# Kernel optimization log

Hardware: AMD Instinct MI355X
Metric: run time of the kernel (lower is better)

The kernel has to match this reference:

```python
import jax, jax.numpy as jnp
import numpy as np

N_HEADS = 16
D_MODEL = 2048
DK = D_MODEL // N_HEADS
SEQ = 2048


def setup_inputs() -> dict:
    key = jax.random.key(0)
    ks = jax.random.split(key, 11)
    s = 0.02
    return {
        "query": jax.random.normal(ks[0], (SEQ, D_MODEL), jnp.float32),
        "key": jax.random.normal(ks[1], (SEQ, D_MODEL), jnp.float32),
        "value": jax.random.normal(ks[2], (SEQ, D_MODEL), jnp.float32),
        # per-head projection weights, stacked over heads: [H, d_model, dk]
        "Wq": jax.random.normal(ks[3], (N_HEADS, D_MODEL, DK), jnp.float32) * s,
        "bq": jnp.zeros((N_HEADS, DK), jnp.float32),
        "Wk": jax.random.normal(ks[4], (N_HEADS, D_MODEL, DK), jnp.float32) * s,
        "bk": jnp.zeros((N_HEADS, DK), jnp.float32),
        "Wv": jax.random.normal(ks[5], (N_HEADS, D_MODEL, DK), jnp.float32) * s,
        "bv": jnp.zeros((N_HEADS, DK), jnp.float32),
        # output projection: [H*dk, d_model]
        "Wo": jax.random.normal(ks[6], (N_HEADS * DK, D_MODEL), jnp.float32) * s,
        "bo": jnp.zeros((D_MODEL,), jnp.float32),
    }


def reference(query, key, value, Wq, bq, Wk, bk, Wv, bv, Wo, bo):
    # Per-head linear projections, batched over heads. q/k/v: [H, S, dk]
    q = jnp.einsum('sd,hdk->hsk', query, Wq) + bq[:, None, :]
    k = jnp.einsum('sd,hdk->hsk', key, Wk) + bk[:, None, :]
    v = jnp.einsum('sd,hdk->hsk', value, Wv) + bv[:, None, :]
    scale = jnp.sqrt(jnp.asarray(DK, q.dtype))
    # scores: [H, S_q, S_k]
    scores = jnp.einsum('hsk,htk->hst', q, k) / scale
    # Faithful to original: Softmax(dim=0) on each 2D [S_q, S_k] matrix
    # -> normalize over the QUERY axis (axis=1 here).
    attn = jax.nn.softmax(scores, axis=1)
    heads = jnp.einsum('hst,htk->hsk', attn, v)  # [H, S, dk]
    # torch.cat(attentions, dim=1): [S, H*dk]
    concat = jnp.transpose(heads, (1, 0, 2)).reshape(SEQ, N_HEADS * DK)
    return concat @ Wo + bo
```

## Files before the change

kernel.cpp:

```cpp
#include <hip/hip_runtime.h>

#define SEQ 2048
#define DMODEL 2048
#define NHEADS 16
#define DKH 128

typedef __bf16 bf16;
typedef __attribute__((ext_vector_type(8))) __bf16 bf16x8;
typedef __attribute__((ext_vector_type(4))) __bf16 bf16x4;
typedef __attribute__((ext_vector_type(4))) float f32x4;

#define AS1 __attribute__((address_space(1)))
#define AS3 __attribute__((address_space(3)))

__device__ __forceinline__ void async_copy16(const void* g, void* l) {
  __builtin_amdgcn_global_load_lds((AS1 void*)(unsigned long long)g,
                                   (AS3 void*)l, 16, 0, 0);
}

__device__ __forceinline__ int swz(int chunk, int row) {
  return (chunk ^ (row & 7)) << 3;
}
__device__ __forceinline__ int swz16(int chunk, int row) {
  return (chunk ^ (row & 15)) << 3;
}

template <typename OutT, bool BIAS>
__global__ __launch_bounds__(256) void gemm_bt(
    const bf16* __restrict__ A, const bf16* __restrict__ B,
    const float* __restrict__ bias, OutT* __restrict__ C,
    int M, int N, int K, int lda, int ldb, int ldo, float scale,
    long long sA, long long sB, long long sC, long long sBias) {
  A += (long long)blockIdx.z * sA;
  B += (long long)blockIdx.z * sB;
  C += (long long)blockIdx.z * sC;
  const float* biasp = BIAS ? (bias + (long long)blockIdx.z * sBias) : nullptr;

  const int m0 = blockIdx.y * 128;
  const int n0 = blockIdx.x * 128;

  __shared__ __align__(16) bf16 As[128 * 64];
  __shared__ __align__(16) bf16 Bs[128 * 64];

  const int tid = threadIdx.x;
  const int wave = tid >> 6;
  const int lane = tid & 63;
  const int srow = wave * 8 + (lane >> 3);
  const int scol = ((lane & 7) ^ (lane >> 3)) * 8;
  const int wr = (wave >> 1) * 64;
  const int wc = (wave & 1) * 64;
  const int lr = lane & 15;
  const int quad = lane >> 4;

  const bf16* ag = A + (long long)(m0 + srow) * lda + scol;
  const bf16* bg = B + (long long)(n0 + srow) * ldb + scol;

  f32x4 acc[4][4];
#pragma unroll
  for (int i = 0; i < 4; ++i)
#pragma unroll
    for (int j = 0; j < 4; ++j) {
      acc[i][j][0] = 0.f; acc[i][j][1] = 0.f;
      acc[i][j][2] = 0.f; acc[i][j][3] = 0.f;
    }

  for (int kt = 0; kt < K; kt += 64) {
#pragma unroll
    for (int i = 0; i < 4; ++i) {
      async_copy16(ag + kt + (long long)i * 32 * lda, As + (i * 32 + wave * 8) * 64);
      async_copy16(bg + kt + (long long)i * 32 * ldb, Bs + (i * 32 + wave * 8) * 64);
    }
    __syncthreads();
#pragma unroll
    for (int kk = 0; kk < 64; kk += 32) {
      bf16x8 af[4], bfr[4];
#pragma unroll
      for (int i = 0; i < 4; ++i) {
        const int ra = wr + i * 16 + lr;
        const int rb = wc + i * 16 + lr;
        af[i]  = *(const bf16x8*)(As + ra * 64 + swz((kk >> 3) + quad, ra));
        bfr[i] = *(const bf16x8*)(Bs + rb * 64 + swz((kk >> 3) + quad, rb));
      }
#pragma unroll
      for (int i = 0; i < 4; ++i)
#pragma unroll
        for (int j = 0; j < 4; ++j)
          acc[i][j] = __builtin_amdgcn_mfma_f32_16x16x32_bf16(af[i], bfr[j], acc[i][j], 0, 0, 0);
    }
    __syncthreads();
  }

#pragma unroll
  for (int j = 0; j < 4; ++j) {
    const int n = n0 + wc + j * 16 + lr;
    const float bv = BIAS ? biasp[n] : 0.f;
#pragma unroll
    for (int i = 0; i < 4; ++i) {
      const int mb = m0 + wr + i * 16 + quad * 4;
#pragma unroll
      for (int r = 0; r < 4; ++r)
        C[(long long)(mb + r) * ldo + n] = (OutT)(acc[i][j][r] * scale + bv);
    }
  }
}

template <typename OutT, bool BIAS>
__global__ __launch_bounds__(256) void gemm_bt64(
    const bf16* __restrict__ A, const bf16* __restrict__ B,
    const float* __restrict__ bias, OutT* __restrict__ C,
    int K, int lda, int ldb, int ldo, float scale,
    long long sA, long long sB, long long sC) {
  A += (long long)blockIdx.z * sA;
  B += (long long)blockIdx.z * sB;
  C += (long long)blockIdx.z * sC;

  const int m0 = blockIdx.y * 64;
  const int n0 = blockIdx.x * 128;

  __shared__ __align__(16) bf16 As[64 * 64];
  __shared__ __align__(16) bf16 Bs[128 * 64];

  const int tid = threadIdx.x;
  const int wave = tid >> 6;
  const int lane = tid & 63;
  const int srow = wave * 8 + (lane >> 3);
  const int scol = ((lane & 7) ^ (lane >> 3)) * 8;
  const int wr = (wave >> 1) * 32;
  const int wc = (wave & 1) * 64;
  const int lr = lane & 15;
  const int quad = lane >> 4;

  const bf16* ag = A + (long long)(m0 + srow) * lda + scol;
  const bf16* bg = B + (long long)(n0 + srow) * ldb + scol;

  f32x4 acc[2][4];
#pragma unroll
  for (int i = 0; i < 2; ++i)
#pragma unroll
    for (int j = 0; j < 4; ++j) {
      acc[i][j][0] = 0.f; acc[i][j][1] = 0.f;
      acc[i][j][2] = 0.f; acc[i][j][3] = 0.f;
    }

  for (int kt = 0; kt < K; kt += 64) {
#pragma unroll
    for (int i = 0; i < 2; ++i)
      async_copy16(ag + kt + (long long)i * 32 * lda, As + (i * 32 + wave * 8) * 64);
#pragma unroll
    for (int i = 0; i < 4; ++i)
      async_copy16(bg + kt + (long long)i * 32 * ldb, Bs + (i * 32 + wave * 8) * 64);
    __syncthreads();
#pragma unroll
    for (int kk = 0; kk < 64; kk += 32) {
      bf16x8 af[2], bfr[4];
#pragma unroll
      for (int i = 0; i < 2; ++i) {
        const int ra = wr + i * 16 + lr;
        af[i] = *(const bf16x8*)(As + ra * 64 + swz((kk >> 3) + quad, ra));
      }
#pragma unroll
      for (int j = 0; j < 4; ++j) {
        const int rb = wc + j * 16 + lr;
        bfr[j] = *(const bf16x8*)(Bs + rb * 64 + swz((kk >> 3) + quad, rb));
      }
#pragma unroll
      for (int i = 0; i < 2; ++i)
#pragma unroll
        for (int j = 0; j < 4; ++j)
          acc[i][j] = __builtin_amdgcn_mfma_f32_16x16x32_bf16(af[i], bfr[j], acc[i][j], 0, 0, 0);
    }
    __syncthreads();
  }

#pragma unroll
  for (int j = 0; j < 4; ++j) {
    const int n = n0 + wc + j * 16 + lr;
    const float bv = BIAS ? bias[n] : 0.f;
#pragma unroll
    for (int i = 0; i < 2; ++i) {
      const int mb = m0 + wr + i * 16 + quad * 4;
#pragma unroll
      for (int r = 0; r < 4; ++r)
        C[(long long)(mb + r) * ldo + n] = (OutT)(acc[i][j][r] * scale + bv);
    }
  }
}

__global__ __launch_bounds__(256) void qk_exp(
    const bf16* __restrict__ q, const bf16* __restrict__ k,
    bf16* __restrict__ E, float* __restrict__ lpart) {
  const int h = blockIdx.z;
  const int m0 = blockIdx.y * 128;
  const int nstrip = blockIdx.x * 512;
  const bf16* A = q + (long long)h * DKH;
  const bf16* B = k + (long long)h * DKH;
  bf16* C = E + (long long)h * SEQ * SEQ;

  __shared__ __align__(16) bf16 As[128 * 128];
  __shared__ __align__(16) bf16 Bs[64 * 128];

  const int tid = threadIdx.x;
  const int wave = tid >> 6;
  const int lane = tid & 63;
  const int wr = (wave >> 1) * 64;
  const int wc = (wave & 1) * 32;
  const int lr = lane & 15;
  const int quad = lane >> 4;
  const float scale = 0.08838834764831845f;

#pragma unroll
  for (int it = 0; it < 8; ++it) {
    const int row = wave * 32 + it * 4 + (lane >> 4);
    const int chunk = (lane & 15) ^ (row & 15);
    async_copy16(A + (long long)(m0 + row) * DMODEL + chunk * 8,
                 As + (wave * 32 + it * 4) * 128);
  }

  for (int nt = 0; nt < 8; ++nt) {
    if (nt) __syncthreads();
#pragma unroll
    for (int it = 0; it < 4; ++it) {
      const int row = wave * 16 + it * 4 + (lane >> 4);
      const int chunk = (lane & 15) ^ (row & 15);
      async_copy16(B + (long long)(nstrip + nt * 64 + row) * DMODEL + chunk * 8,
                   Bs + (wave * 16 + it * 4) * 128);
    }
    __syncthreads();

    f32x4 acc[4][2];
#pragma unroll
    for (int i = 0; i < 4; ++i)
#pragma unroll
      for (int j = 0; j < 2; ++j) {
        acc[i][j][0] = 0.f; acc[i][j][1] = 0.f;
        acc[i][j][2] = 0.f; acc[i][j][3] = 0.f;
      }

#pragma unroll
    for (int kk = 0; kk < 128; kk += 32) {
      bf16x8 af[4], bfr[2];
#pragma unroll
      for (int i = 0; i < 4; ++i) {
        const int ra = wr + i * 16 + lr;
        af[i] = *(const bf16x8*)(As + ra * 128 + swz16((kk >> 3) + quad, ra));
      }
#pragma unroll
      for (int j = 0; j < 2; ++j) {
        const int rb = wc + j * 16 + lr;
        bfr[j] = *(const bf16x8*)(Bs + rb * 128 + swz16((kk >> 3) + quad, rb));
      }
#pragma unroll
      for (int i = 0; i < 4; ++i)
#pragma unroll
        for (int j = 0; j < 2; ++j)
          acc[i][j] = __builtin_amdgcn_mfma_f32_16x16x32_bf16(af[i], bfr[j], acc[i][j], 0, 0, 0);
    }

#pragma unroll
    for (int j = 0; j < 2; ++j) {
      const int n = nstrip + nt * 64 + wc + j * 16 + lr;
      float l_loc = 0.f;
#pragma unroll
      for (int i = 0; i < 4; ++i) {
        const int mb = m0 + wr + i * 16 + quad * 4;
#pragma unroll
        for (int r = 0; r < 4; ++r) {
          bf16 ev = (bf16)__expf(acc[i][j][r] * scale);
          C[(long long)(mb + r) * SEQ + n] = ev;
          l_loc += (float)ev;
        }
      }
      l_loc += __shfl_xor(l_loc, 16, 64);
      l_loc += __shfl_xor(l_loc, 32, 64);
      if (quad == 0)
        lpart[((long long)h * 32 + blockIdx.y * 2 + (wave >> 1)) * SEQ + n] = l_loc;
    }
  }
}

__global__ __launch_bounds__(256) void sum_scale(
    const float* __restrict__ lp, bf16* __restrict__ vt) {
  __shared__ float rv[256];
  const int h = blockIdx.y;
  const int t0 = blockIdx.x * 256;
  const int tid = threadIdx.x;

  float l = 0.f;
#pragma unroll
  for (int rb = 0; rb < 32; ++rb)
    l += lp[((long long)h * 32 + rb) * SEQ + t0 + tid];
  rv[tid] = 1.f / l;
  __syncthreads();

  const int tc = (tid & 31) * 8;
  const int c0 = tid >> 5;
#pragma unroll
  for (int cc = 0; cc < 128; cc += 8) {
    const long long row = (long long)(h * DKH + cc + c0) * SEQ + t0 + tc;
    bf16x8 v = *(const bf16x8*)(vt + row);
#pragma unroll
    for (int e = 0; e < 8; ++e) v[e] = (bf16)((float)v[e] * rv[tc + e]);
    *(bf16x8*)(vt + row) = v;
  }
}

__global__ __launch_bounds__(256) void prep(
    const float* __restrict__ q, const float* __restrict__ k,
    const float* __restrict__ v,
    const float* __restrict__ Wq, const float* __restrict__ Wk,
    const float* __restrict__ Wv, const float* __restrict__ Wo,
    const float* __restrict__ bq, const float* __restrict__ bk,
    const float* __restrict__ bv,
    bf16* __restrict__ Qb, bf16* __restrict__ Wt, bf16* __restrict__ Wot,
    float* __restrict__ biasQKV) {
  __shared__ bf16 t64[64][72];
  const long long elems = (long long)SEQ * DMODEL;
  const int id = blockIdx.x;
  const int tid = threadIdx.x;

  if (id < 12288) {
    const float* src = (id < 4096) ? q : (id < 8192) ? k : v;
    const int t = id >> 12;
    const long long i = (long long)(id & 4095) * 1024 + tid * 4;
    const float4 vv = *(const float4*)(src + i);
    bf16x4 o;
    o[0] = (bf16)vv.x; o[1] = (bf16)vv.y; o[2] = (bf16)vv.z; o[3] = (bf16)vv.w;
    *(bf16x4*)(Qb + (long long)t * elems + i) = o;
    return;
  }
  if (id < 16384) {
    const float* in;
    bf16* o;
    int ldin, c0, r0;
    if (id < 15360) {
      const int rel = id - 12288;
      const int z = rel >> 6;
      const int inner = rel & 63;
      const int g = z >> 4, hh = z & 15;
      in = (g == 0 ? Wq : (g == 1 ? Wk : Wv)) + (long long)hh * DMODEL * DKH;
      o = Wt + (long long)z * DMODEL * DKH;
      ldin = DKH;
      c0 = (inner & 1) * 64;
      r0 = (inner >> 1) * 64;
    } else {
      const int rel = id - 15360;
      in = Wo; o = Wot; ldin = DMODEL;
      c0 = (rel & 31) * 64;
      r0 = (rel >> 5) * 64;
    }
    {
      const int row = tid >> 2;
      const int ch = (tid & 3) * 16;
      const float* src = in + (long long)(r0 + row) * ldin + c0 + ch;
#pragma unroll
      for (int u = 0; u < 4; ++u) {
        const float4 f = *(const float4*)(src + u * 4);
        t64[row][ch + u * 4 + 0] = (bf16)f.x;
        t64[row][ch + u * 4 + 1] = (bf16)f.y;
        t64[row][ch + u * 4 + 2] = (bf16)f.z;
        t64[row][ch + u * 4 + 3] = (bf16)f.w;
      }
    }
    __syncthreads();
    {
      const int oc = tid >> 2;
      const int och = (tid & 3) * 16;
      bf16x8 v0, v1;
#pragma unroll
      for (int e = 0; e < 8; ++e) {
        v0[e] = t64[och + e][oc];
        v1[e] = t64[och + 8 + e][oc];
      }
      bf16* dst = o + (long long)(c0 + oc) * DMODEL + r0 + och;
      *(bf16x8*)dst = v0;
      *(bf16x8*)(dst + 8) = v1;
    }
    return;
  }
  {
    const int i = (id - 16384) * 256 + tid;
    if (i < NHEADS * DKH) {
      biasQKV[i] = bq[i];
      biasQKV[NHEADS * DKH + i] = bk[i];
      biasQKV[2 * NHEADS * DKH + i] = bv[i];
    }
  }
}

__global__ __launch_bounds__(256) void transpose_v(
    const bf16* __restrict__ in, bf16* __restrict__ out) {
  __shared__ bf16 tile[64][72];
  const int c0 = blockIdx.x * 64, r0 = blockIdx.y * 64;
  const int tid = threadIdx.x;
  const int row = tid >> 3;
  const int ch = (tid & 7) * 8;
#pragma unroll
  for (int p = 0; p < 2; ++p) {
    const int r = row + p * 32;
    *(bf16x8*)(&tile[r][ch]) =
        *(const bf16x8*)(in + (long long)(r0 + r) * DMODEL + c0 + ch);
  }
  __syncthreads();
#pragma unroll
  for (int p = 0; p < 2; ++p) {
    const int c = row + p * 32;
    bf16x8 v;
#pragma unroll
    for (int e = 0; e < 8; ++e) v[e] = tile[ch + e][c];
    *(bf16x8*)(out + (long long)(c0 + c) * SEQ + r0 + ch) = v;
  }
}

extern "C" void kernel_launch(void* const* d_in, const int* in_sizes, int n_in,
                              void* d_out, int out_size, void* d_ws, size_t ws_size,
                              hipStream_t stream) {
  const float* query = (const float*)d_in[0];
  const float* key_  = (const float*)d_in[1];
  const float* value = (const float*)d_in[2];
  const float* Wq = (const float*)d_in[3];
  const float* bq = (const float*)d_in[4];
  const float* Wk = (const float*)d_in[5];
  const float* bk = (const float*)d_in[6];
  const float* Wv = (const float*)d_in[7];
  const float* bv = (const float*)d_in[8];
  const float* Wo = (const float*)d_in[9];
  const float* bo = (const float*)d_in[10];
  float* out = (float*)d_out;

  const long long elems = (long long)SEQ * DMODEL;
  const long long SZB = elems * 2;

  char* ws = (char*)d_ws;
  bf16* Qb = (bf16*)ws;
  bf16* Wt = (bf16*)(ws + 3 * SZB);
  bf16* scores = (bf16*)ws;
  char* p = ws + (long long)NHEADS * SEQ * SEQ * 2;
  float* biasQKV = (float*)p; p += 32 * 1024;
  bf16* Wot   = (bf16*)p; p += SZB;
  bf16* qkv   = (bf16*)p; p += 3 * SZB;
  bf16* vt    = (bf16*)p; p += SZB;
  bf16* heads = (bf16*)p; p += SZB;
  float* lpart = (float*)p; p += (long long)NHEADS * 32 * SEQ * 4;
  if ((size_t)(p - ws) > ws_size) return;

  prep<<<16392, 256, 0, stream>>>(query, key_, value, Wq, Wk, Wv, Wo,
                                  bq, bk, bv, Qb, Wt, Wot, biasQKV);

  gemm_bt<bf16, true><<<dim3(16, 16, 3), 256, 0, stream>>>(
      Qb, Wt, biasQKV, qkv, SEQ, DMODEL, DMODEL, DMODEL, DMODEL, DMODEL, 1.f,
      elems, elems, elems, (long long)DMODEL);

  transpose_v<<<dim3(DMODEL / 64, SEQ / 64), 256, 0, stream>>>(
      qkv + 2 * elems, vt);

  qk_exp<<<dim3(4, 16, NHEADS), 256, 0, stream>>>(qkv, qkv + elems, scores, lpart);

  sum_scale<<<dim3(SEQ / 256, NHEADS), 256, 0, stream>>>(lpart, vt);

  gemm_bt64<bf16, false><<<dim3(1, SEQ / 64, NHEADS), 256, 0, stream>>>(
      scores, vt, nullptr, heads, SEQ, SEQ, SEQ, DMODEL, 1.f,
      (long long)SEQ * SEQ, (long long)DKH * SEQ, (long long)DKH);

  gemm_bt64<float, true><<<dim3(DMODEL / 128, SEQ / 64, 1), 256, 0, stream>>>(
      heads, Wot, bo, out, DMODEL, DMODEL, DMODEL, DMODEL, 1.f, 0, 0, 0);
}
```

Before: 340.3 us.

## Stage exp scores through LDS for coalesced stores and remap GEMM block order

```diff
diff --git a/kernel.cpp b/kernel.cpp
--- a/kernel.cpp
+++ b/kernel.cpp
@@ -31,13 +31,19 @@
     const float* __restrict__ bias, OutT* __restrict__ C,
     int M, int N, int K, int lda, int ldb, int ldo, float scale,
     long long sA, long long sB, long long sC, long long sBias) {
-  A += (long long)blockIdx.z * sA;
-  B += (long long)blockIdx.z * sB;
-  C += (long long)blockIdx.z * sC;
-  const float* biasp = BIAS ? (bias + (long long)blockIdx.z * sBias) : nullptr;
-
-  const int m0 = blockIdx.y * 128;
-  const int n0 = blockIdx.x * 128;
+  const int gx = gridDim.x, gxy = gridDim.x * gridDim.y;
+  const int nwg = gxy * gridDim.z;
+  int flat = blockIdx.x + gx * blockIdx.y + gxy * blockIdx.z;
+  flat = (flat & 7) * (nwg >> 3) + (flat >> 3);
+  const int bz = flat / gxy;
+  const int rem = flat - bz * gxy;
+  const int m0 = (rem / gx) * 128;
+  const int n0 = (rem % gx) * 128;
+
+  A += (long long)bz * sA;
+  B += (long long)bz * sB;
+  C += (long long)bz * sC;
+  const float* biasp = BIAS ? (bias + (long long)bz * sBias) : nullptr;
 
   __shared__ __align__(16) bf16 As[128 * 64];
   __shared__ __align__(16) bf16 Bs[128 * 64];
@@ -256,17 +262,24 @@
           acc[i][j] = __builtin_amdgcn_mfma_f32_16x16x32_bf16(af[i], bfr[j], acc[i][j], 0, 0, 0);
     }
 
+    __syncthreads();
+
+    bf16* Es = Bs;
 #pragma unroll
     for (int j = 0; j < 2; ++j) {
-      const int n = nstrip + nt * 64 + wc + j * 16 + lr;
+      const int col = wc + j * 16 + lr;
+      const int n = nstrip + nt * 64 + col;
+      const int chunk = col >> 3;
+      const int cw = col & 7;
       float l_loc = 0.f;
 #pragma unroll
       for (int i = 0; i < 4; ++i) {
-        const int mb = m0 + wr + i * 16 + quad * 4;
+        const int row0 = wr + i * 16 + quad * 4;
 #pragma unroll
         for (int r = 0; r < 4; ++r) {
+          const int row = row0 + r;
           bf16 ev = (bf16)__expf(acc[i][j][r] * scale);
-          C[(long long)(mb + r) * SEQ + n] = ev;
+          Es[row * 64 + ((chunk ^ (((row >> 2) & 3) << 1)) << 3) + cw] = ev;
           l_loc += (float)ev;
         }
       }
@@ -274,6 +287,20 @@
       l_loc += __shfl_xor(l_loc, 32, 64);
       if (quad == 0)
         lpart[((long long)h * 32 + blockIdx.y * 2 + (wave >> 1)) * SEQ + n] = l_loc;
+    }
+    __syncthreads();
+
+    {
+      const int erow = tid >> 1;
+      const int ecb = (tid & 1) * 4;
+      const int es = ((erow >> 2) & 3) << 1;
+      bf16* dst = C + (long long)(m0 + erow) * SEQ + nstrip + nt * 64;
+#pragma unroll
+      for (int u = 0; u < 4; ++u) {
+        const int ch = ecb + u;
+        *(bf16x8*)(dst + ch * 8) =
+            *(const bf16x8*)(Es + erow * 64 + ((ch ^ es) << 3));
+      }
     }
   }
 }
```

Result: slower. 357.5 us (+5.0%).
